# Kernel optimization log

Hardware: AMD Instinct MI355X
Metric: run time of the kernel (lower is better)

The kernel has to match this reference:

```python
import jax, jax.numpy as jnp
import numpy as np

H = 256  # hidden size
I = 2    # input size / output size


def setup_inputs() -> dict:
    key = jax.random.key(0)
    ks = jax.random.split(key, 11)
    s1 = 1.0 / np.sqrt(H)
    u = lambda k, shape: jax.random.uniform(k, shape, jnp.float32, -s1, s1)
    return {
        "inputs": jax.random.normal(ks[0], (512, 256, I), jnp.float32),
        "W_ih1": u(ks[1], (4 * H, I)),
        "W_hh1": u(ks[2], (4 * H, H)),
        "b_ih1": u(ks[3], (4 * H,)),
        "b_hh1": u(ks[4], (4 * H,)),
        "W_ih2": u(ks[5], (4 * H, H)),
        "W_hh2": u(ks[6], (4 * H, H)),
        "b_ih2": u(ks[7], (4 * H,)),
        "b_hh2": u(ks[8], (4 * H,)),
        "W_lin": u(ks[9], (I, H)),
        "b_lin": u(ks[10], (I,)),
    }


def _lstm_cell(x, h, c, W_ih, W_hh, b_ih, b_hh):
    # PyTorch LSTMCell gate order: i, f, g, o
    gates = x @ W_ih.T + b_ih + h @ W_hh.T + b_hh  # (B, 4H)
    i, f, g, o = jnp.split(gates, 4, axis=-1)
    c_new = jax.nn.sigmoid(f) * c + jax.nn.sigmoid(i) * jnp.tanh(g)
    h_new = jax.nn.sigmoid(o) * jnp.tanh(c_new)
    return h_new, c_new


def reference(inputs, W_ih1, W_hh1, b_ih1, b_hh1, W_ih2, W_hh2, b_ih2, b_hh2,
              W_lin, b_lin):
    B = inputs.shape[0]
    xs = jnp.transpose(inputs, (1, 0, 2))  # (T, B, I)
    zeros = jnp.zeros((B, H), inputs.dtype)
    carry0 = (zeros, zeros, zeros, zeros)

    def step(carry, x_t):
        h1, c1, h2, c2 = carry
        # NOTE: the original clones/masks x_t into lstm_input_t but never
        # uses it — the cell consumes raw input_t, so we do the same.
        h1, c1 = _lstm_cell(x_t, h1, c1, W_ih1, W_hh1, b_ih1, b_hh1)
        h2, c2 = _lstm_cell(h1, h2, c2, W_ih2, W_hh2, b_ih2, b_hh2)
        y = h2 @ W_lin.T + b_lin  # (B, I)
        return (h1, c1, h2, c2), y

    _, ys = jax.lax.scan(step, carry0, xs)  # ys: (T, B, I)
    return jnp.transpose(ys, (1, 0, 2))  # (B, T, I)
```

## Files before the change

kernel.cpp:

```cpp
#include <hip/hip_runtime.h>


typedef float vf2 __attribute__((ext_vector_type(2)));
typedef _Float16 vh2 __attribute__((ext_vector_type(2)));
typedef _Float16 vh4 __attribute__((ext_vector_type(4)));
typedef _Float16 vh8 __attribute__((ext_vector_type(8)));

#define NT 512
#define TSTEPS 256
#define NCH 96
#define NSTRM 88
#define CHB 16384
#define FS 393216

__global__ void prep_kernel(const float* __restrict__ W_ih1,
                            const float* __restrict__ W_hh1,
                            const float* __restrict__ b_ih1,
                            const float* __restrict__ b_hh1,
                            const float* __restrict__ W_ih2,
                            const float* __restrict__ W_hh2,
                            const float* __restrict__ b_ih2,
                            const float* __restrict__ b_hh2,
                            void* __restrict__ ws) {
    const int stride = gridDim.x * blockDim.x;
    const int idx = blockIdx.x * blockDim.x + threadIdx.x;
    _Float16* wh = (_Float16*)ws;
    float* wf = (float*)ws;
    for (int e = idx; e < NCH * 8192; e += stride) {
        int ch = e >> 13, rem = e & 8191;
        int th = rem >> 4, r = (rem >> 3) & 1, i = rem & 7;
        int row = th + (r << 9);
        int k = (ch << 3) + i;
        float v;
        if (k < 256)      v = W_hh1[row * 256 + k];
        else if (k < 512) v = W_ih2[row * 256 + (k - 256)];
        else              v = W_hh2[row * 256 + (k - 512)];
        wh[e] = (_Float16)v;
    }
    for (int j = idx; j < 1024; j += stride) {
        wf[FS + j]        = W_ih1[j * 2 + 0];
        wf[FS + 1024 + j] = W_ih1[j * 2 + 1];
        wf[FS + 2048 + j] = b_ih1[j] + b_hh1[j];
        wf[FS + 3072 + j] = b_ih2[j] + b_hh2[j];
    }
}

__device__ __forceinline__ float sig_(float v) {
    return 1.f / (1.f + __expf(-v));
}
__device__ __forceinline__ float tanh_(float v) {
    return 1.f - 2.f / (__expf(2.f * v) + 1.f);
}
__device__ __forceinline__ float fdot2_(vh2 a, vh2 b, float c) {
#if __has_builtin(__builtin_amdgcn_fdot2)
    return __builtin_amdgcn_fdot2(a, b, c, false);
#else
    return c + (float)a.x * (float)b.x + (float)a.y * (float)b.y;
#endif
}

union W8 { vh8 v; vh2 p[4]; };
struct WPair { vh8 r0, r1; };

#define BARRIER() __asm__ volatile("s_waitcnt lgkmcnt(0)\ns_barrier" ::: "memory")

__global__ __launch_bounds__(NT, 2) void lstm_kernel(
    const float* __restrict__ x,
    const void* __restrict__ ws,
    const float* __restrict__ W_lin,
    const float* __restrict__ b_lin,
    float* __restrict__ out)
{
    __shared__ float gbuf[2][1024];
    __shared__ _Float16 hl1[2][2][256];
    __shared__ _Float16 hl2[2][2][256];
    __shared__ char lds_park[8][CHB];

    const int tid = threadIdx.x;
    const int j = tid;
    const int u = tid & 255, bu = tid >> 8;
    const int b0 = blockIdx.x * 2;
    const char* wstream = (const char*)ws;
    const float* wf = (const float*)ws;

    const float wx0a = wf[FS + j],        wx1a = wf[FS + 1024 + j];
    const float wx0b = wf[FS + 512 + j],  wx1b = wf[FS + 1536 + j];
    const float bj1a = wf[FS + 2048 + j], bj1b = wf[FS + 2560 + j];
    const float bj2a = wf[FS + 3072 + j], bj2b = wf[FS + 3584 + j];

    const int lane = tid & 63, wv = tid >> 6;
    const int ob = (wv >> 1) & 1, oo = wv & 1;
    const float wl0 = W_lin[oo * 256 + 4 * lane + 0];
    const float wl1 = W_lin[oo * 256 + 4 * lane + 1];
    const float wl2 = W_lin[oo * 256 + 4 * lane + 2];
    const float wl3 = W_lin[oo * 256 + 4 * lane + 3];
    const float blin = b_lin[oo];

    for (int i = tid; i < 2 * 2 * 256; i += NT) {
        ((_Float16*)hl1)[i] = (_Float16)0.f;
        ((_Float16*)hl2)[i] = (_Float16)0.f;
    }

    float c1 = 0.f, c2 = 0.f;
    vf2 xv0 = *(const vf2*)(x + (size_t)(b0 + 0) * 512);
    vf2 xv1 = *(const vf2*)(x + (size_t)(b0 + 1) * 512);

    const int t32 = tid * 32;
    int sp = 0;
    float a00, a01, a10, a11;

    auto loadc = [&](WPair& d) {
        d.r0 = *(const vh8*)(wstream + sp + t32);
        d.r1 = *(const vh8*)(wstream + sp + t32 + 16);
        sp += CHB;
        if (sp == NSTRM * CHB) sp = 0;
    };
    auto usec = [&](const WPair& w, const _Float16 (*hp)[256], int k0) {
        W8 u0; u0.v = w.r0;
        W8 u1; u1.v = w.r1;
        W8 ha; ha.v = *(const vh8*)&hp[0][k0];
        W8 hb; hb.v = *(const vh8*)&hp[1][k0];
        a00 = fdot2_(u0.p[0], ha.p[0], a00); a00 = fdot2_(u0.p[1], ha.p[1], a00);
        a00 = fdot2_(u0.p[2], ha.p[2], a00); a00 = fdot2_(u0.p[3], ha.p[3], a00);
        a01 = fdot2_(u0.p[0], hb.p[0], a01); a01 = fdot2_(u0.p[1], hb.p[1], a01);
        a01 = fdot2_(u0.p[2], hb.p[2], a01); a01 = fdot2_(u0.p[3], hb.p[3], a01);
        a10 = fdot2_(u1.p[0], ha.p[0], a10); a10 = fdot2_(u1.p[1], ha.p[1], a10);
        a10 = fdot2_(u1.p[2], ha.p[2], a10); a10 = fdot2_(u1.p[3], ha.p[3], a10);
        a11 = fdot2_(u1.p[0], hb.p[0], a11); a11 = fdot2_(u1.p[1], hb.p[1], a11);
        a11 = fdot2_(u1.p[2], hb.p[2], a11); a11 = fdot2_(u1.p[3], hb.p[3], a11);
    };

    for (int s = 0; s < 8; ++s) {
        const char* src = wstream + (size_t)(88 + s) * CHB + t32;
        *(vh8*)&lds_park[s][t32]      = *(const vh8*)src;
        *(vh8*)&lds_park[s][t32 + 16] = *(const vh8*)(src + 16);
    }

    WPair bA, bB, bC, bD;
    loadc(bA); loadc(bB); loadc(bC); loadc(bD);
    __syncthreads();

    auto gemm32 = [&](const _Float16 (*hp)[256]) {
        #pragma unroll 1
        for (int q = 0; q < 32; q += 4) {
            usec(bA, hp, 8 * q);      loadc(bA);
            usec(bB, hp, 8 * q + 8);  loadc(bB);
            usec(bC, hp, 8 * q + 16); loadc(bC);
            usec(bD, hp, 8 * q + 24); loadc(bD);
        }
    };
    auto gemm24 = [&](const _Float16 (*hp)[256]) {
        #pragma unroll 1
        for (int q = 0; q < 24; q += 4) {
            usec(bA, hp, 8 * q);      loadc(bA);
            usec(bB, hp, 8 * q + 8);  loadc(bB);
            usec(bC, hp, 8 * q + 16); loadc(bC);
            usec(bD, hp, 8 * q + 24); loadc(bD);
        }
    };

    #pragma unroll 1
    for (int t = 0; t < TSTEPS; ++t) {
        const int p = t & 1, pm = p ^ 1;

        a00 = bj1a + wx0a * xv0.x + wx1a * xv0.y;
        a01 = bj1a + wx0a * xv1.x + wx1a * xv1.y;
        a10 = bj1b + wx0b * xv0.x + wx1b * xv0.y;
        a11 = bj1b + wx0b * xv1.x + wx1b * xv1.y;
        gemm32(hl1[pm]);
        gbuf[0][j] = a00; gbuf[1][j] = a01;
        gbuf[0][512 + j] = a10; gbuf[1][512 + j] = a11;
        BARRIER();

        {
            float gi = sig_(gbuf[bu][u]);
            float gf = sig_(gbuf[bu][256 + u]);
            float gg = tanh_(gbuf[bu][512 + u]);
            float go = sig_(gbuf[bu][768 + u]);
            c1 = gf * c1 + gi * gg;
            hl1[p][bu][u] = (_Float16)(go * tanh_(c1));
        }
        BARRIER();

        a00 = bj2a; a01 = bj2a; a10 = bj2b; a11 = bj2b;
        gemm32(hl1[p]);
        gemm24(hl2[pm]);
        {
            const _Float16 (*hp)[256] = hl2[pm];
            #pragma unroll 1
            for (int s = 0; s < 8; ++s) {
                WPair w;
                w.r0 = *(const vh8*)&lds_park[s][t32];
                w.r1 = *(const vh8*)&lds_park[s][t32 + 16];
                usec(w, hp, 192 + 8 * s);
            }
        }
        gbuf[0][j] = a00; gbuf[1][j] = a01;
        gbuf[0][512 + j] = a10; gbuf[1][512 + j] = a11;
        BARRIER();

        {
            float gi = sig_(gbuf[bu][u]);
            float gf = sig_(gbuf[bu][256 + u]);
            float gg = tanh_(gbuf[bu][512 + u]);
            float go = sig_(gbuf[bu][768 + u]);
            c2 = gf * c2 + gi * gg;
            hl2[p][bu][u] = (_Float16)(go * tanh_(c2));
        }
        BARRIER();

        if (wv < 4) {
            vh4 hv = *(const vh4*)&hl2[p][ob][4 * lane];
            float s = (float)hv.x * wl0 + (float)hv.y * wl1
                    + (float)hv.z * wl2 + (float)hv.w * wl3;
            #pragma unroll
            for (int m = 32; m >= 1; m >>= 1) s += __shfl_xor(s, m, 64);
            if (lane == 0)
                out[(size_t)(b0 + ob) * 512 + t * 2 + oo] = s + blin;
        }

        const int tn = (t + 1) & (TSTEPS - 1);
        xv0 = *(const vf2*)(x + (size_t)(b0 + 0) * 512 + tn * 2);
        xv1 = *(const vf2*)(x + (size_t)(b0 + 1) * 512 + tn * 2);
    }
}

extern "C" void kernel_launch(void* const* d_in, const int* in_sizes, int n_in,
                              void* d_out, int out_size, void* d_ws, size_t ws_size,
                              hipStream_t stream) {
    const float* x     = (const float*)d_in[0];
    const float* W_ih1 = (const float*)d_in[1];
    const float* W_hh1 = (const float*)d_in[2];
    const float* b_ih1 = (const float*)d_in[3];
    const float* b_hh1 = (const float*)d_in[4];
    const float* W_ih2 = (const float*)d_in[5];
    const float* W_hh2 = (const float*)d_in[6];
    const float* b_ih2 = (const float*)d_in[7];
    const float* b_hh2 = (const float*)d_in[8];
    const float* W_lin = (const float*)d_in[9];
    const float* b_lin = (const float*)d_in[10];
    float* out = (float*)d_out;

    prep_kernel<<<256, 256, 0, stream>>>(W_ih1, W_hh1, b_ih1, b_hh1,
                                         W_ih2, W_hh2, b_ih2, b_hh2, d_ws);
    lstm_kernel<<<256, NT, 0, stream>>>(x, d_ws, W_lin, b_lin, out);
}
```

Before: 3.281 ms.

## Skew layer-1 and layer-2 recurrences to halve per-step barriers

Restructures the time loop so layer 1's gate GEMM for step t+1 runs in the same phase as layer 2's GEMM for step t. Each step now has two block barriers instead of four, and the double-buffered hidden-state arrays become single buffers. Gate buffers are split per layer, the final output is written after the loop, and the input load is prefetched two steps ahead. The parked-in-LDS weight chunks are re-laid out so each thread reads 16-byte contiguous slices from two halves, which is meant to reduce LDS bank conflicts. In exchange the code relies on subtler ordering between the barriers and the shared buffers.

```diff
diff --git a/kernel.cpp b/kernel.cpp
--- a/kernel.cpp
+++ b/kernel.cpp
@@ -28,7 +28,9 @@
     float* wf = (float*)ws;
     for (int e = idx; e < NCH * 8192; e += stride) {
         int ch = e >> 13, rem = e & 8191;
-        int th = rem >> 4, r = (rem >> 3) & 1, i = rem & 7;
+        int th, r, i;
+        if (ch >= NSTRM) { r = rem >> 12; th = (rem >> 3) & 511; i = rem & 7; }
+        else             { th = rem >> 4; r = (rem >> 3) & 1;    i = rem & 7; }
         int row = th + (r << 9);
         int k = (ch << 3) + i;
         float v;
@@ -71,9 +73,10 @@
     const float* __restrict__ b_lin,
     float* __restrict__ out)
 {
-    __shared__ float gbuf[2][1024];
-    __shared__ _Float16 hl1[2][2][256];
-    __shared__ _Float16 hl2[2][2][256];
+    __shared__ float g1buf[2][1024];
+    __shared__ float g2buf[2][1024];
+    __shared__ _Float16 h1s[2][256];
+    __shared__ _Float16 h2s[2][256];
     __shared__ char lds_park[8][CHB];
 
     const int tid = threadIdx.x;
@@ -96,18 +99,13 @@
     const float wl3 = W_lin[oo * 256 + 4 * lane + 3];
     const float blin = b_lin[oo];
 
-    for (int i = tid; i < 2 * 2 * 256; i += NT) {
-        ((_Float16*)hl1)[i] = (_Float16)0.f;
-        ((_Float16*)hl2)[i] = (_Float16)0.f;
-    }
+    ((_Float16*)h1s)[tid] = (_Float16)0.f;
+    ((_Float16*)h2s)[tid] = (_Float16)0.f;
 
     float c1 = 0.f, c2 = 0.f;
-    vf2 xv0 = *(const vf2*)(x + (size_t)(b0 + 0) * 512);
-    vf2 xv1 = *(const vf2*)(x + (size_t)(b0 + 1) * 512);
-
-    const int t32 = tid * 32;
+
+    const int t16 = tid * 16, t32 = tid * 32;
     int sp = 0;
-    float a00, a01, a10, a11;
 
     auto loadc = [&](WPair& d) {
         d.r0 = *(const vh8*)(wstream + sp + t32);
@@ -115,113 +113,132 @@
         sp += CHB;
         if (sp == NSTRM * CHB) sp = 0;
     };
-    auto usec = [&](const WPair& w, const _Float16 (*hp)[256], int k0) {
+    auto usec = [&](const WPair& w, const _Float16 (*hp)[256], int k0,
+                    float& A00, float& A01, float& A10, float& A11) {
         W8 u0; u0.v = w.r0;
         W8 u1; u1.v = w.r1;
         W8 ha; ha.v = *(const vh8*)&hp[0][k0];
         W8 hb; hb.v = *(const vh8*)&hp[1][k0];
-        a00 = fdot2_(u0.p[0], ha.p[0], a00); a00 = fdot2_(u0.p[1], ha.p[1], a00);
-        a00 = fdot2_(u0.p[2], ha.p[2], a00); a00 = fdot2_(u0.p[3], ha.p[3], a00);
-        a01 = fdot2_(u0.p[0], hb.p[0], a01); a01 = fdot2_(u0.p[1], hb.p[1], a01);
-        a01 = fdot2_(u0.p[2], hb.p[2], a01); a01 = fdot2_(u0.p[3], hb.p[3], a01);
-        a10 = fdot2_(u1.p[0], ha.p[0], a10); a10 = fdot2_(u1.p[1], ha.p[1], a10);
-        a10 = fdot2_(u1.p[2], ha.p[2], a10); a10 = fdot2_(u1.p[3], ha.p[3], a10);
-        a11 = fdot2_(u1.p[0], hb.p[0], a11); a11 = fdot2_(u1.p[1], hb.p[1], a11);
-        a11 = fdot2_(u1.p[2], hb.p[2], a11); a11 = fdot2_(u1.p[3], hb.p[3], a11);
+        A00 = fdot2_(u0.p[0], ha.p[0], A00); A00 = fdot2_(u0.p[1], ha.p[1], A00);
+        A00 = fdot2_(u0.p[2], ha.p[2], A00); A00 = fdot2_(u0.p[3], ha.p[3], A00);
+        A01 = fdot2_(u0.p[0], hb.p[0], A01); A01 = fdot2_(u0.p[1], hb.p[1], A01);
+        A01 = fdot2_(u0.p[2], hb.p[2], A01); A01 = fdot2_(u0.p[3], hb.p[3], A01);
+        A10 = fdot2_(u1.p[0], ha.p[0], A10); A10 = fdot2_(u1.p[1], ha.p[1], A10);
+        A10 = fdot2_(u1.p[2], ha.p[2], A10); A10 = fdot2_(u1.p[3], ha.p[3], A10);
+        A11 = fdot2_(u1.p[0], hb.p[0], A11); A11 = fdot2_(u1.p[1], hb.p[1], A11);
+        A11 = fdot2_(u1.p[2], hb.p[2], A11); A11 = fdot2_(u1.p[3], hb.p[3], A11);
     };
 
     for (int s = 0; s < 8; ++s) {
-        const char* src = wstream + (size_t)(88 + s) * CHB + t32;
-        *(vh8*)&lds_park[s][t32]      = *(const vh8*)src;
-        *(vh8*)&lds_park[s][t32 + 16] = *(const vh8*)(src + 16);
-    }
+        const char* src = wstream + (size_t)(NSTRM + s) * CHB;
+        *(vh8*)&lds_park[s][t16]        = *(const vh8*)(src + t16);
+        *(vh8*)&lds_park[s][8192 + t16] = *(const vh8*)(src + 8192 + t16);
+    }
+
+    {
+        vf2 x0a = *(const vf2*)(x + (size_t)(b0 + 0) * 512);
+        vf2 x0b = *(const vf2*)(x + (size_t)(b0 + 1) * 512);
+        g1buf[0][j]       = bj1a + wx0a * x0a.x + wx1a * x0a.y;
+        g1buf[1][j]       = bj1a + wx0a * x0b.x + wx1a * x0b.y;
+        g1buf[0][512 + j] = bj1b + wx0b * x0a.x + wx1b * x0a.y;
+        g1buf[1][512 + j] = bj1b + wx0b * x0b.x + wx1b * x0b.y;
+    }
+    vf2 xv0 = *(const vf2*)(x + (size_t)(b0 + 0) * 512 + 2);
+    vf2 xv1 = *(const vf2*)(x + (size_t)(b0 + 1) * 512 + 2);
 
     WPair bA, bB, bC, bD;
     loadc(bA); loadc(bB); loadc(bC); loadc(bD);
     __syncthreads();
 
-    auto gemm32 = [&](const _Float16 (*hp)[256]) {
+    auto gemm32 = [&](const _Float16 (*hp)[256],
+                      float& A00, float& A01, float& A10, float& A11) {
         #pragma unroll 1
         for (int q = 0; q < 32; q += 4) {
-            usec(bA, hp, 8 * q);      loadc(bA);
-            usec(bB, hp, 8 * q + 8);  loadc(bB);
-            usec(bC, hp, 8 * q + 16); loadc(bC);
-            usec(bD, hp, 8 * q + 24); loadc(bD);
-        }
-    };
-    auto gemm24 = [&](const _Float16 (*hp)[256]) {
+            usec(bA, hp, 8 * q,      A00, A01, A10, A11); loadc(bA);
+            usec(bB, hp, 8 * q + 8,  A00, A01, A10, A11); loadc(bB);
+            usec(bC, hp, 8 * q + 16, A00, A01, A10, A11); loadc(bC);
+            usec(bD, hp, 8 * q + 24, A00, A01, A10, A11); loadc(bD);
+        }
+    };
+    auto gemm24 = [&](const _Float16 (*hp)[256],
+                      float& A00, float& A01, float& A10, float& A11) {
         #pragma unroll 1
         for (int q = 0; q < 24; q += 4) {
-            usec(bA, hp, 8 * q);      loadc(bA);
-            usec(bB, hp, 8 * q + 8);  loadc(bB);
-            usec(bC, hp, 8 * q + 16); loadc(bC);
-            usec(bD, hp, 8 * q + 24); loadc(bD);
+            usec(bA, hp, 8 * q,      A00, A01, A10, A11); loadc(bA);
+            usec(bB, hp, 8 * q + 8,  A00, A01, A10, A11); loadc(bB);
+            usec(bC, hp, 8 * q + 16, A00, A01, A10, A11); loadc(bC);
+            usec(bD, hp, 8 * q + 24, A00, A01, A10, A11); loadc(bD);
         }
     };
 
     #pragma unroll 1
     for (int t = 0; t < TSTEPS; ++t) {
-        const int p = t & 1, pm = p ^ 1;
-
-        a00 = bj1a + wx0a * xv0.x + wx1a * xv0.y;
-        a01 = bj1a + wx0a * xv1.x + wx1a * xv1.y;
-        a10 = bj1b + wx0b * xv0.x + wx1b * xv0.y;
-        a11 = bj1b + wx0b * xv1.x + wx1b * xv1.y;
-        gemm32(hl1[pm]);
-        gbuf[0][j] = a00; gbuf[1][j] = a01;
-        gbuf[0][512 + j] = a10; gbuf[1][512 + j] = a11;
+        {
+            float gi = sig_(g1buf[bu][u]);
+            float gf = sig_(g1buf[bu][256 + u]);
+            float gg = tanh_(g1buf[bu][512 + u]);
+            float go = sig_(g1buf[bu][768 + u]);
+            c1 = gf * c1 + gi * gg;
+            h1s[bu][u] = (_Float16)(go * tanh_(c1));
+        }
         BARRIER();
 
-        {
-            float gi = sig_(gbuf[bu][u]);
-            float gf = sig_(gbuf[bu][256 + u]);
-            float gg = tanh_(gbuf[bu][512 + u]);
-            float go = sig_(gbuf[bu][768 + u]);
-            c1 = gf * c1 + gi * gg;
-            hl1[p][bu][u] = (_Float16)(go * tanh_(c1));
-        }
-        BARRIER();
-
-        a00 = bj2a; a01 = bj2a; a10 = bj2b; a11 = bj2b;
-        gemm32(hl1[p]);
-        gemm24(hl2[pm]);
-        {
-            const _Float16 (*hp)[256] = hl2[pm];
-            #pragma unroll 1
-            for (int s = 0; s < 8; ++s) {
-                WPair w;
-                w.r0 = *(const vh8*)&lds_park[s][t32];
-                w.r1 = *(const vh8*)&lds_park[s][t32 + 16];
-                usec(w, hp, 192 + 8 * s);
-            }
-        }
-        gbuf[0][j] = a00; gbuf[1][j] = a01;
-        gbuf[0][512 + j] = a10; gbuf[1][512 + j] = a11;
-        BARRIER();
-
-        {
-            float gi = sig_(gbuf[bu][u]);
-            float gf = sig_(gbuf[bu][256 + u]);
-            float gg = tanh_(gbuf[bu][512 + u]);
-            float go = sig_(gbuf[bu][768 + u]);
-            c2 = gf * c2 + gi * gg;
-            hl2[p][bu][u] = (_Float16)(go * tanh_(c2));
-        }
-        BARRIER();
-
-        if (wv < 4) {
-            vh4 hv = *(const vh4*)&hl2[p][ob][4 * lane];
+        if (t > 0 && wv < 4) {
+            vh4 hv = *(const vh4*)&h2s[ob][4 * lane];
             float s = (float)hv.x * wl0 + (float)hv.y * wl1
                     + (float)hv.z * wl2 + (float)hv.w * wl3;
             #pragma unroll
             for (int m = 32; m >= 1; m >>= 1) s += __shfl_xor(s, m, 64);
             if (lane == 0)
-                out[(size_t)(b0 + ob) * 512 + t * 2 + oo] = s + blin;
-        }
-
-        const int tn = (t + 1) & (TSTEPS - 1);
-        xv0 = *(const vf2*)(x + (size_t)(b0 + 0) * 512 + tn * 2);
-        xv1 = *(const vf2*)(x + (size_t)(b0 + 1) * 512 + tn * 2);
+                out[(size_t)(b0 + ob) * 512 + (t - 1) * 2 + oo] = s + blin;
+        }
+
+        float a00 = bj1a + wx0a * xv0.x + wx1a * xv0.y;
+        float a01 = bj1a + wx0a * xv1.x + wx1a * xv1.y;
+        float a10 = bj1b + wx0b * xv0.x + wx1b * xv0.y;
+        float a11 = bj1b + wx0b * xv1.x + wx1b * xv1.y;
+        {
+            const int tn = (t + 2) & (TSTEPS - 1);
+            xv0 = *(const vf2*)(x + (size_t)(b0 + 0) * 512 + tn * 2);
+            xv1 = *(const vf2*)(x + (size_t)(b0 + 1) * 512 + tn * 2);
+        }
+        gemm32(h1s, a00, a01, a10, a11);
+        g1buf[0][j] = a00; g1buf[1][j] = a01;
+        g1buf[0][512 + j] = a10; g1buf[1][512 + j] = a11;
+
+        a00 = bj2a; a01 = bj2a; a10 = bj2b; a11 = bj2b;
+        gemm32(h1s, a00, a01, a10, a11);
+        gemm24(h2s, a00, a01, a10, a11);
+        #pragma unroll 1
+        for (int s = 0; s < 8; ++s) {
+            WPair w;
+            w.r0 = *(const vh8*)&lds_park[s][t16];
+            w.r1 = *(const vh8*)&lds_park[s][8192 + t16];
+            usec(w, h2s, 192 + 8 * s, a00, a01, a10, a11);
+        }
+        g2buf[0][j] = a00; g2buf[1][j] = a01;
+        g2buf[0][512 + j] = a10; g2buf[1][512 + j] = a11;
+        BARRIER();
+
+        {
+            float gi = sig_(g2buf[bu][u]);
+            float gf = sig_(g2buf[bu][256 + u]);
+            float gg = tanh_(g2buf[bu][512 + u]);
+            float go = sig_(g2buf[bu][768 + u]);
+            c2 = gf * c2 + gi * gg;
+            h2s[bu][u] = (_Float16)(go * tanh_(c2));
+        }
+    }
+
+    BARRIER();
+    if (wv < 4) {
+        vh4 hv = *(const vh4*)&h2s[ob][4 * lane];
+        float s = (float)hv.x * wl0 + (float)hv.y * wl1
+                + (float)hv.z * wl2 + (float)hv.w * wl3;
+        #pragma unroll
+        for (int m = 32; m >= 1; m >>= 1) s += __shfl_xor(s, m, 64);
+        if (lane == 0)
+            out[(size_t)(b0 + ob) * 512 + 255 * 2 + oo] = s + blin;
     }
 }
 
```

After: 3.315 ms. Within noise of the previous version (+1.0%).
